# Kernel optimization log

Hardware: AMD Instinct MI355X
Metric: run time of the kernel (lower is better)

Reference implementation:

```python
import jax, jax.numpy as jnp
import numpy as np

NEG_SLOPE = 0.2
EPS = 0.0  # default eps, non-trainable buffer
N_NODES = 50000
N_EDGES = 400000
D = 512  # state_dim


def setup_inputs() -> dict:
    key = jax.random.key(0)
    ks = jax.random.split(key, 8)
    x = jax.random.normal(ks[0], (N_NODES, D), dtype=jnp.float32)
    row = jax.random.randint(ks[1], (N_EDGES,), 0, N_NODES)
    col = jax.random.randint(ks[2], (N_EDGES,), 0, N_NODES)
    # remove_self_loops: guarantee no self loops at data-gen time (static shapes)
    col = jnp.where(row == col, (col + 1) % N_NODES, col)
    edge_index = jnp.stack([row, col], axis=0)  # [2, E]
    condition = jax.random.normal(ks[3], (1, 256), dtype=jnp.float32)
    scale = 1.0 / np.sqrt(256.0)
    Wk = jax.random.normal(ks[4], (256, 2 * D), dtype=jnp.float32) * scale
    W1 = jax.random.normal(ks[5], (D, 2 * D), dtype=jnp.float32) / np.sqrt(D)
    b1 = jnp.zeros((2 * D,), dtype=jnp.float32)
    W2 = jax.random.normal(ks[6], (2 * D, D), dtype=jnp.float32) / np.sqrt(2 * D)
    b2 = jnp.zeros((D,), dtype=jnp.float32)
    return {"x": x, "edge_index": edge_index, "condition": condition,
            "Wk": Wk, "W1": W1, "b1": b1, "W2": W2, "b2": b2}


def reference(x, edge_index, condition, Wk, W1, b1, W2, b2):
    row, col = edge_index[0], edge_index[1]
    key = condition @ Wk                      # [1, 2D]
    ki, kj = key[0, :D], key[0, D:]           # x_i pairs with first half, x_j with second
    x_i = x[col]                              # [E, D]
    # alpha = (cat([x_i, x_j]) * key).sum(-1) without materializing the concat
    alpha = x_i @ ki + x[row] @ kj            # [E]
    alpha = jnp.where(alpha >= 0, alpha, NEG_SLOPE * alpha)  # leaky_relu
    alpha = jax.nn.sigmoid(alpha)
    agg = jax.ops.segment_sum(x_i * alpha[:, None], row, num_segments=x.shape[0])
    out = (1.0 + EPS) * x + agg
    out = jax.nn.relu(out @ W1 + b1) @ W2 + b2  # h_Theta MLP
    return out
```

## Files before the change

kernel.cpp:

```cpp
#include <hip/hip_runtime.h>

#define D 512
#define H1 1024
#define NNODES 50000
#define NEDGES 400000
#define MPAD 50048
#define NEG_SLOPE 0.2f
#define SCAN_BLOCKS 196

typedef __attribute__((ext_vector_type(8))) short bf16x8;
typedef __attribute__((ext_vector_type(8))) unsigned short u16x8;
typedef __attribute__((ext_vector_type(4))) float f32x4;


__device__ __forceinline__ unsigned short f2bf(float f) {
  unsigned int u = __float_as_uint(f);
  unsigned int r = u + 0x7FFFu + ((u >> 16) & 1u);
  return (unsigned short)(r >> 16);
}
__device__ __forceinline__ float bf2f(unsigned short h) {
  return __uint_as_float((unsigned int)h << 16);
}

__device__ __forceinline__ void gl_lds16(const void* g, void* l) {
  __builtin_amdgcn_global_load_lds(
      (const __attribute__((address_space(1))) void*)g,
      (__attribute__((address_space(3))) void*)l, 16, 0, 0);
}

__global__ void key_kernel(const float* __restrict__ cond, const float* __restrict__ Wk,
                           float* __restrict__ key) {
  int j = blockIdx.x * blockDim.x + threadIdx.x;
  if (j >= 2 * D) return;
  float s = 0.f;
#pragma unroll 8
  for (int i = 0; i < 256; ++i) s += cond[i] * Wk[i * (2 * D) + j];
  key[j] = s;
}

__global__ void nodedot_kernel(const float* __restrict__ x, const float* __restrict__ key,
                               float* __restrict__ nki, float* __restrict__ nkj,
                               unsigned short* __restrict__ xb) {
  int wid = (blockIdx.x * blockDim.x + threadIdx.x) >> 6;
  int lane = threadIdx.x & 63;
  if (wid >= NNODES) return;
  const float4* xr = (const float4*)(x + (size_t)wid * D);
  float4 p0 = xr[2 * lane], p1 = xr[2 * lane + 1];
  const float4* kia = (const float4*)key;
  const float4* kja = (const float4*)(key + D);
  float4 q0 = kia[2 * lane], q1 = kia[2 * lane + 1];
  float4 r0 = kja[2 * lane], r1 = kja[2 * lane + 1];
  float a = p0.x * q0.x + p0.y * q0.y + p0.z * q0.z + p0.w * q0.w +
            p1.x * q1.x + p1.y * q1.y + p1.z * q1.z + p1.w * q1.w;
  float b = p0.x * r0.x + p0.y * r0.y + p0.z * r0.z + p0.w * r0.w +
            p1.x * r1.x + p1.y * r1.y + p1.z * r1.z + p1.w * r1.w;
  u16x8 h;
  h[0] = f2bf(p0.x); h[1] = f2bf(p0.y); h[2] = f2bf(p0.z); h[3] = f2bf(p0.w);
  h[4] = f2bf(p1.x); h[5] = f2bf(p1.y); h[6] = f2bf(p1.z); h[7] = f2bf(p1.w);
  *(u16x8*)(xb + (size_t)wid * D + 8 * lane) = h;
#pragma unroll
  for (int off = 32; off > 0; off >>= 1) {
    a += __shfl_xor(a, off);
    b += __shfl_xor(b, off);
  }
  if (lane == 0) { nki[wid] = a; nkj[wid] = b; }
}

__global__ void convw_kernel(const float* __restrict__ W1, const float* __restrict__ W2,
                             unsigned short* __restrict__ W1t, unsigned short* __restrict__ W2t) {
  int idx = blockIdx.x * blockDim.x + threadIdx.x;
  if (idx >= D * H1) return;
  {
    int k = idx / H1, n = idx % H1;
    size_t a = (((size_t)(n >> 7) * (D >> 3) + (k >> 3)) << 10) + ((n & 127) << 3) + (k & 7);
    W1t[a] = f2bf(W1[idx]);
  }
  {
    int k = idx / D, n = idx % D;
    size_t a = (((size_t)(n >> 7) * (H1 >> 3) + (k >> 3)) << 10) + ((n & 127) << 3) + (k & 7);
    W2t[a] = f2bf(W2[idx]);
  }
}

__global__ void zero_deg_kernel(int* __restrict__ deg) {
  int i = blockIdx.x * blockDim.x + threadIdx.x;
  if (i < NNODES) deg[i] = 0;
}

__global__ void hist_kernel(const int* __restrict__ row, int* __restrict__ deg) {
  int e = blockIdx.x * blockDim.x + threadIdx.x;
  if (e < NEDGES) atomicAdd(&deg[row[e]], 1);
}

__global__ void scan1_kernel(const int* __restrict__ deg, int* __restrict__ rowptr,
                             int* __restrict__ blktot) {
  __shared__ int s[256];
  int tid = threadIdx.x;
  int i = blockIdx.x * 256 + tid;
  int v = (i < NNODES) ? deg[i] : 0;
  s[tid] = v;
  __syncthreads();
#pragma unroll
  for (int off = 1; off < 256; off <<= 1) {
    int t = (tid >= off) ? s[tid - off] : 0;
    __syncthreads();
    s[tid] += t;
    __syncthreads();
  }
  if (i < NNODES) rowptr[i] = s[tid] - v;
  if (tid == 255) blktot[blockIdx.x] = s[255];
}

__global__ void scan2_kernel(int* __restrict__ blktot, int* __restrict__ blkoff) {
  __shared__ int s[256];
  int tid = threadIdx.x;
  int v = (tid < SCAN_BLOCKS) ? blktot[tid] : 0;
  s[tid] = v;
  __syncthreads();
#pragma unroll
  for (int off = 1; off < 256; off <<= 1) {
    int t = (tid >= off) ? s[tid - off] : 0;
    __syncthreads();
    s[tid] += t;
    __syncthreads();
  }
  if (tid < SCAN_BLOCKS) blkoff[tid] = s[tid] - v;
}

__global__ void scan3_kernel(int* __restrict__ rowptr, const int* __restrict__ blkoff,
                             int* __restrict__ cursor) {
  int i = blockIdx.x * blockDim.x + threadIdx.x;
  if (i < NNODES) {
    int v = rowptr[i] + blkoff[blockIdx.x];
    rowptr[i] = v;
    cursor[i] = v;
  }
  if (i == 0) rowptr[NNODES] = NEDGES;
}

__global__ void fill_kernel(const int* __restrict__ row, const int* __restrict__ col,
                            const float* __restrict__ nki, const float* __restrict__ nkj,
                            int* __restrict__ cursor, int* __restrict__ scol,
                            float* __restrict__ salpha) {
  int e = blockIdx.x * blockDim.x + threadIdx.x;
  if (e >= NEDGES) return;
  int r = row[e], c = col[e];
  float a = nki[c] + nkj[r];
  a = (a >= 0.f) ? a : NEG_SLOPE * a;
  float al = 1.f / (1.f + expf(-a));
  int pos = atomicAdd(&cursor[r], 1);
  scol[pos] = c;
  salpha[pos] = al;
}

__global__ __launch_bounds__(256) void agg_kernel(
    const unsigned short* __restrict__ xb, const int* __restrict__ rowptr,
    const int* __restrict__ scol, const float* __restrict__ salpha,
    unsigned short* __restrict__ Pb) {
  int n = (blockIdx.x * blockDim.x + threadIdx.x) >> 6;
  int lane = threadIdx.x & 63;
  if (n >= NNODES) return;
  int beg = rowptr[n], end = rowptr[n + 1];
  u16x8 self = *(const u16x8*)(xb + (size_t)n * D + 8 * lane);
  float sa[8], sb[8];
#pragma unroll
  for (int q = 0; q < 8; ++q) { sa[q] = bf2f(self[q]); sb[q] = 0.f; }
  int e = beg;
  for (; e + 1 < end; e += 2) {
    int c0 = scol[e], c1 = scol[e + 1];
    float al0 = salpha[e], al1 = salpha[e + 1];
    u16x8 w0 = *(const u16x8*)(xb + (size_t)c0 * D + 8 * lane);
    u16x8 w1 = *(const u16x8*)(xb + (size_t)c1 * D + 8 * lane);
#pragma unroll
    for (int q = 0; q < 8; ++q) {
      sa[q] += al0 * bf2f(w0[q]);
      sb[q] += al1 * bf2f(w1[q]);
    }
  }
  if (e < end) {
    int c0 = scol[e];
    float al0 = salpha[e];
    u16x8 w0 = *(const u16x8*)(xb + (size_t)c0 * D + 8 * lane);
#pragma unroll
    for (int q = 0; q < 8; ++q) sa[q] += al0 * bf2f(w0[q]);
  }
  u16x8 h;
#pragma unroll
  for (int q = 0; q < 8; ++q) h[q] = f2bf(sa[q] + sb[q]);
  *(u16x8*)(Pb + (((size_t)(n >> 7) * (D >> 3) + lane) << 10) + ((n & 127) << 3)) = h;
}

template <bool RELU_OUT_BF16>
__global__ __launch_bounds__(256) void gemm_kernel(
    const unsigned short* __restrict__ Ag, const unsigned short* __restrict__ Bt,
    const float* __restrict__ bias, void* __restrict__ Cptr, int M_valid, int K, int N) {
  __shared__ unsigned short As[8 * 128 * 8];
  __shared__ unsigned short Bs[8 * 128 * 8];

  const int G = gridDim.x * gridDim.y;
  const int orig = blockIdx.y * gridDim.x + blockIdx.x;
  const int qq = G >> 3, rr = G & 7;
  const int xcd = orig & 7, loc = orig >> 3;
  const int wg = (xcd < rr ? xcd * (qq + 1) : rr * (qq + 1) + (xcd - rr) * qq) + loc;
  const int bx = wg % gridDim.x;
  const int by = wg / gridDim.x;

  const int tid = threadIdx.x;
  const int lane = tid & 63;
  const int wave = tid >> 6;
  const int wm = (wave >> 1) * 64;
  const int wn = (wave & 1) * 64;
  const int n0 = bx * 128;
  const int fr = lane & 15;
  const int kq = lane >> 4;

  const unsigned short* Apan = Ag + ((size_t)by * (K >> 3) << 10);
  const unsigned short* Bpan = Bt + ((size_t)bx * (K >> 3) << 10);

  f32x4 acc[4][4];
#pragma unroll
  for (int i = 0; i < 4; ++i)
#pragma unroll
    for (int j = 0; j < 4; ++j)
#pragma unroll
      for (int r = 0; r < 4; ++r) acc[i][j][r] = 0.f;

  for (int k0 = 0; k0 < K; k0 += 64) {
#pragma unroll
    for (int ss = 0; ss < 4; ++ss) {
      int s = wave * 4 + ss;
      int rbase = (s & 1) * 64;
      int kca = (k0 >> 3) + (s >> 1);
      gl_lds16(Apan + ((size_t)kca << 10) + (rbase + lane) * 8, &As[s * 512]);
      gl_lds16(Bpan + ((size_t)kca << 10) + (rbase + lane) * 8, &Bs[s * 512]);
    }
    __syncthreads();

#pragma unroll
    for (int h = 0; h < 2; ++h) {
      const int kc = h * 4 + kq;
      bf16x8 af[4], bfr[4];
#pragma unroll
      for (int i = 0; i < 4; ++i)
        af[i] = *(const bf16x8*)&As[(kc * 128 + wm + i * 16 + fr) * 8];
#pragma unroll
      for (int j = 0; j < 4; ++j)
        bfr[j] = *(const bf16x8*)&Bs[(kc * 128 + wn + j * 16 + fr) * 8];
#pragma unroll
      for (int i = 0; i < 4; ++i)
#pragma unroll
        for (int j = 0; j < 4; ++j)
          acc[i][j] = __builtin_amdgcn_mfma_f32_16x16x32_bf16(af[i], bfr[j], acc[i][j], 0, 0, 0);
    }
    __syncthreads();
  }

  const int rg = kq * 4;
#pragma unroll
  for (int i = 0; i < 4; ++i) {
#pragma unroll
    for (int j = 0; j < 4; ++j) {
      int gn = n0 + wn + j * 16 + fr;
      float bv = bias[gn];
#pragma unroll
      for (int r = 0; r < 4; ++r) {
        int lr = wm + i * 16 + rg + r;
        float v = acc[i][j][r] + bv;
        if constexpr (RELU_OUT_BF16) {
          v = fmaxf(v, 0.f);
          size_t a = (((size_t)by * (N >> 3) + (gn >> 3)) << 10) + (lr << 3) + (gn & 7);
          ((unsigned short*)Cptr)[a] = f2bf(v);
        } else {
          int gm = by * 128 + lr;
          if (gm < M_valid) ((float*)Cptr)[(size_t)gm * N + gn] = v;
        }
      }
    }
  }
}

extern "C" void kernel_launch(void* const* d_in, const int* in_sizes, int n_in,
                              void* d_out, int out_size, void* d_ws, size_t ws_size,
                              hipStream_t stream) {
  const float* x    = (const float*)d_in[0];
  const int*   ei   = (const int*)d_in[1];
  const float* cond = (const float*)d_in[2];
  const float* Wk   = (const float*)d_in[3];
  const float* W1   = (const float*)d_in[4];
  const float* b1   = (const float*)d_in[5];
  const float* W2   = (const float*)d_in[6];
  const float* b2   = (const float*)d_in[7];
  float* out = (float*)d_out;

  char* ws = (char*)d_ws;
  size_t off = 0;
  auto alloc = [&](size_t b) { size_t p = off; off += (b + 255) & ~(size_t)255; return p; };
  float* key = (float*)(ws + alloc(2 * D * sizeof(float)));
  float* nki = (float*)(ws + alloc(NNODES * sizeof(float)));
  float* nkj = (float*)(ws + alloc(NNODES * sizeof(float)));
  int* deg    = (int*)(ws + alloc(NNODES * sizeof(int)));
  int* rowptr = (int*)(ws + alloc((NNODES + 1) * sizeof(int)));
  int* cursor = (int*)(ws + alloc(NNODES * sizeof(int)));
  int* blktot = (int*)(ws + alloc(SCAN_BLOCKS * sizeof(int)));
  int* blkoff = (int*)(ws + alloc(SCAN_BLOCKS * sizeof(int)));
  int* scol      = (int*)(ws + alloc(NEDGES * sizeof(int)));
  float* salpha  = (float*)(ws + alloc(NEDGES * sizeof(float)));
  unsigned short* xb  = (unsigned short*)(ws + alloc((size_t)NNODES * D * 2));
  unsigned short* W1t = (unsigned short*)(ws + alloc((size_t)H1 * D * 2));
  unsigned short* W2t = (unsigned short*)(ws + alloc((size_t)D * H1 * 2));
  unsigned short* Pb  = (unsigned short*)(ws + alloc((size_t)MPAD * D * 2));
  unsigned short* Hb  = (unsigned short*)(ws + alloc((size_t)MPAD * H1 * 2));

  const int* row = ei;
  const int* col = ei + NEDGES;

  key_kernel<<<dim3((2 * D + 255) / 256), dim3(256), 0, stream>>>(cond, Wk, key);
  nodedot_kernel<<<dim3(NNODES * 64 / 256), dim3(256), 0, stream>>>(x, key, nki, nkj, xb);
  convw_kernel<<<dim3(D * H1 / 256), dim3(256), 0, stream>>>(W1, W2, W1t, W2t);

  zero_deg_kernel<<<dim3(SCAN_BLOCKS), dim3(256), 0, stream>>>(deg);
  hist_kernel<<<dim3((NEDGES + 255) / 256), dim3(256), 0, stream>>>(row, deg);
  scan1_kernel<<<dim3(SCAN_BLOCKS), dim3(256), 0, stream>>>(deg, rowptr, blktot);
  scan2_kernel<<<dim3(1), dim3(256), 0, stream>>>(blktot, blkoff);
  scan3_kernel<<<dim3(SCAN_BLOCKS), dim3(256), 0, stream>>>(rowptr, blkoff, cursor);
  fill_kernel<<<dim3((NEDGES + 255) / 256), dim3(256), 0, stream>>>(row, col, nki, nkj,
                                                                    cursor, scol, salpha);
  agg_kernel<<<dim3(NNODES * 64 / 256 + 1), dim3(256), 0, stream>>>(xb, rowptr, scol, salpha, Pb);

  gemm_kernel<true><<<dim3(H1 / 128, MPAD / 128), dim3(256), 0, stream>>>(
      Pb, W1t, b1, Hb, NNODES, D, H1);
  gemm_kernel<false><<<dim3(D / 128, MPAD / 128), dim3(256), 0, stream>>>(
      Hb, W2t, b2, out, NNODES, H1, D);
}
```

Before: 360.6 us.

## Fuse prep kernels into one launch and compute edge alpha inside aggregation

Merges the node-dot/bf16 convert, weight conversion and degree histogram into a single block-partitioned prep kernel, and replaces the zero kernel with a memset. Edge attention weights are now computed on the fly in the aggregation kernel from per-node dot products, which removes the salpha array and its write/read traffic. MPAD grows to 50176 (a multiple of 256), which adds more padded rows to the GEMM grids. Per-edge sigmoid work moves into the agg loop, where it sits next to the gathers.

```diff
diff --git a/kernel.cpp b/kernel.cpp
--- a/kernel.cpp
+++ b/kernel.cpp
@@ -4,13 +4,18 @@
 #define H1 1024
 #define NNODES 50000
 #define NEDGES 400000
-#define MPAD 50048
+#define MPAD 50176
 #define NEG_SLOPE 0.2f
 #define SCAN_BLOCKS 196
+
+#define NB_ND 12500
+#define NB_CW 2048
+#define NB_HI 1563
 
 typedef __attribute__((ext_vector_type(8))) short bf16x8;
 typedef __attribute__((ext_vector_type(8))) unsigned short u16x8;
 typedef __attribute__((ext_vector_type(4))) float f32x4;
+typedef __attribute__((ext_vector_type(4))) unsigned int u32x4;
 
 
 __device__ __forceinline__ unsigned short f2bf(float f) {
@@ -38,58 +43,54 @@
   key[j] = s;
 }
 
-__global__ void nodedot_kernel(const float* __restrict__ x, const float* __restrict__ key,
-                               float* __restrict__ nki, float* __restrict__ nkj,
-                               unsigned short* __restrict__ xb) {
-  int wid = (blockIdx.x * blockDim.x + threadIdx.x) >> 6;
-  int lane = threadIdx.x & 63;
-  if (wid >= NNODES) return;
-  const float4* xr = (const float4*)(x + (size_t)wid * D);
-  float4 p0 = xr[2 * lane], p1 = xr[2 * lane + 1];
-  const float4* kia = (const float4*)key;
-  const float4* kja = (const float4*)(key + D);
-  float4 q0 = kia[2 * lane], q1 = kia[2 * lane + 1];
-  float4 r0 = kja[2 * lane], r1 = kja[2 * lane + 1];
-  float a = p0.x * q0.x + p0.y * q0.y + p0.z * q0.z + p0.w * q0.w +
-            p1.x * q1.x + p1.y * q1.y + p1.z * q1.z + p1.w * q1.w;
-  float b = p0.x * r0.x + p0.y * r0.y + p0.z * r0.z + p0.w * r0.w +
-            p1.x * r1.x + p1.y * r1.y + p1.z * r1.z + p1.w * r1.w;
-  u16x8 h;
-  h[0] = f2bf(p0.x); h[1] = f2bf(p0.y); h[2] = f2bf(p0.z); h[3] = f2bf(p0.w);
-  h[4] = f2bf(p1.x); h[5] = f2bf(p1.y); h[6] = f2bf(p1.z); h[7] = f2bf(p1.w);
-  *(u16x8*)(xb + (size_t)wid * D + 8 * lane) = h;
-#pragma unroll
-  for (int off = 32; off > 0; off >>= 1) {
-    a += __shfl_xor(a, off);
-    b += __shfl_xor(b, off);
-  }
-  if (lane == 0) { nki[wid] = a; nkj[wid] = b; }
-}
-
-__global__ void convw_kernel(const float* __restrict__ W1, const float* __restrict__ W2,
-                             unsigned short* __restrict__ W1t, unsigned short* __restrict__ W2t) {
-  int idx = blockIdx.x * blockDim.x + threadIdx.x;
-  if (idx >= D * H1) return;
-  {
-    int k = idx / H1, n = idx % H1;
-    size_t a = (((size_t)(n >> 7) * (D >> 3) + (k >> 3)) << 10) + ((n & 127) << 3) + (k & 7);
-    W1t[a] = f2bf(W1[idx]);
-  }
-  {
-    int k = idx / D, n = idx % D;
-    size_t a = (((size_t)(n >> 7) * (H1 >> 3) + (k >> 3)) << 10) + ((n & 127) << 3) + (k & 7);
-    W2t[a] = f2bf(W2[idx]);
-  }
-}
-
-__global__ void zero_deg_kernel(int* __restrict__ deg) {
-  int i = blockIdx.x * blockDim.x + threadIdx.x;
-  if (i < NNODES) deg[i] = 0;
-}
-
-__global__ void hist_kernel(const int* __restrict__ row, int* __restrict__ deg) {
-  int e = blockIdx.x * blockDim.x + threadIdx.x;
-  if (e < NEDGES) atomicAdd(&deg[row[e]], 1);
+__global__ __launch_bounds__(256) void prep_kernel(
+    const float* __restrict__ x, const float* __restrict__ key,
+    const float* __restrict__ W1, const float* __restrict__ W2,
+    const int* __restrict__ row,
+    float* __restrict__ nki, float* __restrict__ nkj, unsigned short* __restrict__ xb,
+    unsigned short* __restrict__ W1t, unsigned short* __restrict__ W2t,
+    int* __restrict__ deg) {
+  const int b = blockIdx.x;
+  const int tid = threadIdx.x;
+  if (b < NB_ND) {
+    int wid = (b * 256 + tid) >> 6;
+    int lane = tid & 63;
+    const float4* xr = (const float4*)(x + (size_t)wid * D);
+    float4 p0 = xr[2 * lane], p1 = xr[2 * lane + 1];
+    const float4* kia = (const float4*)key;
+    const float4* kja = (const float4*)(key + D);
+    float4 q0 = kia[2 * lane], q1 = kia[2 * lane + 1];
+    float4 r0 = kja[2 * lane], r1 = kja[2 * lane + 1];
+    float a = p0.x * q0.x + p0.y * q0.y + p0.z * q0.z + p0.w * q0.w +
+              p1.x * q1.x + p1.y * q1.y + p1.z * q1.z + p1.w * q1.w;
+    float bb = p0.x * r0.x + p0.y * r0.y + p0.z * r0.z + p0.w * r0.w +
+               p1.x * r1.x + p1.y * r1.y + p1.z * r1.z + p1.w * r1.w;
+    u16x8 h;
+    h[0] = f2bf(p0.x); h[1] = f2bf(p0.y); h[2] = f2bf(p0.z); h[3] = f2bf(p0.w);
+    h[4] = f2bf(p1.x); h[5] = f2bf(p1.y); h[6] = f2bf(p1.z); h[7] = f2bf(p1.w);
+    *(u16x8*)(xb + (size_t)wid * D + 8 * lane) = h;
+#pragma unroll
+    for (int off = 32; off > 0; off >>= 1) {
+      a += __shfl_xor(a, off);
+      bb += __shfl_xor(bb, off);
+    }
+    if (lane == 0) { nki[wid] = a; nkj[wid] = bb; }
+  } else if (b < NB_ND + NB_CW) {
+    int idx = (b - NB_ND) * 256 + tid;
+    {
+      int k = idx / H1, n = idx % H1;
+      size_t a = (((size_t)(n >> 7) * (D >> 3) + (k >> 3)) << 10) + ((n & 127) << 3) + (k & 7);
+      W1t[a] = f2bf(W1[idx]);
+    }
+    {
+      int k = idx / D, n = idx % D;
+      size_t a = (((size_t)(n >> 7) * (H1 >> 3) + (k >> 3)) << 10) + ((n & 127) << 3) + (k & 7);
+      W2t[a] = f2bf(W2[idx]);
+    }
+  } else {
+    int e = (b - NB_ND - NB_CW) * 256 + tid;
+    if (e < NEDGES) atomicAdd(&deg[row[e]], 1);
+  }
 }
 
 __global__ void scan1_kernel(const int* __restrict__ deg, int* __restrict__ rowptr,
@@ -139,38 +140,37 @@
 }
 
 __global__ void fill_kernel(const int* __restrict__ row, const int* __restrict__ col,
-                            const float* __restrict__ nki, const float* __restrict__ nkj,
-                            int* __restrict__ cursor, int* __restrict__ scol,
-                            float* __restrict__ salpha) {
+                            int* __restrict__ cursor, int* __restrict__ scol) {
   int e = blockIdx.x * blockDim.x + threadIdx.x;
   if (e >= NEDGES) return;
-  int r = row[e], c = col[e];
-  float a = nki[c] + nkj[r];
-  a = (a >= 0.f) ? a : NEG_SLOPE * a;
-  float al = 1.f / (1.f + expf(-a));
-  int pos = atomicAdd(&cursor[r], 1);
-  scol[pos] = c;
-  salpha[pos] = al;
+  int pos = atomicAdd(&cursor[row[e]], 1);
+  scol[pos] = col[e];
 }
 
 __global__ __launch_bounds__(256) void agg_kernel(
     const unsigned short* __restrict__ xb, const int* __restrict__ rowptr,
-    const int* __restrict__ scol, const float* __restrict__ salpha,
-    unsigned short* __restrict__ Pb) {
+    const int* __restrict__ scol, const float* __restrict__ nki,
+    const float* __restrict__ nkj, unsigned short* __restrict__ Pb) {
   int n = (blockIdx.x * blockDim.x + threadIdx.x) >> 6;
   int lane = threadIdx.x & 63;
   if (n >= NNODES) return;
   int beg = rowptr[n], end = rowptr[n + 1];
+  const float nkjn = nkj[n];
   u16x8 self = *(const u16x8*)(xb + (size_t)n * D + 8 * lane);
   float sa[8], sb[8];
 #pragma unroll
   for (int q = 0; q < 8; ++q) { sa[q] = bf2f(self[q]); sb[q] = 0.f; }
+  auto alpha = [&](int c) {
+    float a = nki[c] + nkjn;
+    a = (a >= 0.f) ? a : NEG_SLOPE * a;
+    return 1.f / (1.f + expf(-a));
+  };
   int e = beg;
   for (; e + 1 < end; e += 2) {
     int c0 = scol[e], c1 = scol[e + 1];
-    float al0 = salpha[e], al1 = salpha[e + 1];
     u16x8 w0 = *(const u16x8*)(xb + (size_t)c0 * D + 8 * lane);
     u16x8 w1 = *(const u16x8*)(xb + (size_t)c1 * D + 8 * lane);
+    float al0 = alpha(c0), al1 = alpha(c1);
 #pragma unroll
     for (int q = 0; q < 8; ++q) {
       sa[q] += al0 * bf2f(w0[q]);
@@ -179,8 +179,8 @@
   }
   if (e < end) {
     int c0 = scol[e];
-    float al0 = salpha[e];
     u16x8 w0 = *(const u16x8*)(xb + (size_t)c0 * D + 8 * lane);
+    float al0 = alpha(c0);
 #pragma unroll
     for (int q = 0; q < 8; ++q) sa[q] += al0 * bf2f(w0[q]);
   }
@@ -304,7 +304,6 @@
   int* blktot = (int*)(ws + alloc(SCAN_BLOCKS * sizeof(int)));
   int* blkoff = (int*)(ws + alloc(SCAN_BLOCKS * sizeof(int)));
   int* scol      = (int*)(ws + alloc(NEDGES * sizeof(int)));
-  float* salpha  = (float*)(ws + alloc(NEDGES * sizeof(float)));
   unsigned short* xb  = (unsigned short*)(ws + alloc((size_t)NNODES * D * 2));
   unsigned short* W1t = (unsigned short*)(ws + alloc((size_t)H1 * D * 2));
   unsigned short* W2t = (unsigned short*)(ws + alloc((size_t)D * H1 * 2));
@@ -314,18 +313,16 @@
   const int* row = ei;
   const int* col = ei + NEDGES;
 
-  key_kernel<<<dim3((2 * D + 255) / 256), dim3(256), 0, stream>>>(cond, Wk, key);
-  nodedot_kernel<<<dim3(NNODES * 64 / 256), dim3(256), 0, stream>>>(x, key, nki, nkj, xb);
-  convw_kernel<<<dim3(D * H1 / 256), dim3(256), 0, stream>>>(W1, W2, W1t, W2t);
-
-  zero_deg_kernel<<<dim3(SCAN_BLOCKS), dim3(256), 0, stream>>>(deg);
-  hist_kernel<<<dim3((NEDGES + 255) / 256), dim3(256), 0, stream>>>(row, deg);
+  hipMemsetAsync(deg, 0, NNODES * sizeof(int), stream);
+  key_kernel<<<dim3(4), dim3(256), 0, stream>>>(cond, Wk, key);
+  prep_kernel<<<dim3(NB_ND + NB_CW + NB_HI), dim3(256), 0, stream>>>(
+      x, key, W1, W2, row, nki, nkj, xb, W1t, W2t, deg);
+
   scan1_kernel<<<dim3(SCAN_BLOCKS), dim3(256), 0, stream>>>(deg, rowptr, blktot);
   scan2_kernel<<<dim3(1), dim3(256), 0, stream>>>(blktot, blkoff);
   scan3_kernel<<<dim3(SCAN_BLOCKS), dim3(256), 0, stream>>>(rowptr, blkoff, cursor);
-  fill_kernel<<<dim3((NEDGES + 255) / 256), dim3(256), 0, stream>>>(row, col, nki, nkj,
-                                                                    cursor, scol, salpha);
-  agg_kernel<<<dim3(NNODES * 64 / 256 + 1), dim3(256), 0, stream>>>(xb, rowptr, scol, salpha, Pb);
+  fill_kernel<<<dim3((NEDGES + 255) / 256), dim3(256), 0, stream>>>(row, col, cursor, scol);
+  agg_kernel<<<dim3(NB_ND), dim3(256), 0, stream>>>(xb, rowptr, scol, nki, nkj, Pb);
 
   gemm_kernel<true><<<dim3(H1 / 128, MPAD / 128), dim3(256), 0, stream>>>(
       Pb, W1t, b1, Hb, NNODES, D, H1);
```

After: 364.2 us. Within noise of the previous version (+1.0%).
